# Optimization experiments

Hardware: AMD Instinct MI355X
Metric: run time of the kernel (lower is better)

Reference implementation:

```python
import jax, jax.numpy as jnp
import numpy as np
from jax import lax

B, T, C = 64, 1024, 256


def setup_inputs() -> dict:
    key = jax.random.key(0)
    k1, k2 = jax.random.split(key)
    sequences = jax.random.normal(k1, (B, T, C), dtype=jnp.float32)
    transitions = jax.random.normal(k2, (C, C), dtype=jnp.float32)
    return {"sequences": sequences, "transitions": transitions}


def _viterbi_decode(sequences, transitions):
    # sequences: [B, T, C] unary scores; transitions: [C_prev, C_cur]
    num_classes = sequences.shape[-1]
    emissions = jnp.swapaxes(sequences, 0, 1)  # [T, B, C]

    def fwd_step(alpha, emit):
        # alpha: [B, C_prev]; emit: [B, C_cur]
        m = alpha[:, :, None] + transitions[None, :, :]  # [B, C_prev, C_cur]
        bp = jnp.argmax(m, axis=1).astype(jnp.int32)     # [B, C_cur] backpointers
        new_alpha = jnp.max(m, axis=1) + emit            # [B, C_cur]
        return new_alpha, bp

    alpha, bps = lax.scan(fwd_step, emissions[0], emissions[1:])  # bps: [T-1, B, C]
    last_tag = jnp.argmax(alpha, axis=-1).astype(jnp.int32)       # [B]

    def back_step(tag, bp):
        # tag: [B] tag at t+1; bp: [B, C] backpointers computed at step t+1
        prev = jnp.take_along_axis(bp, tag[:, None], axis=1)[:, 0]
        return prev, prev

    _, tags = lax.scan(back_step, last_tag, bps, reverse=True)  # [T-1, B]
    full = jnp.concatenate([tags, last_tag[None, :]], axis=0)   # [T, B]
    return jnp.swapaxes(full, 0, 1)  # [B, T]


def reference(sequences, transitions):
    # Inference path of CRF.call: viterbi decode + one-hot over num_classes.
    tags = _viterbi_decode(sequences, transitions)
    return jax.nn.one_hot(tags, sequences.shape[-1], dtype=sequences.dtype)
```

## Files before the change

kernel.cpp:

```cpp
#include <hip/hip_runtime.h>

#define Bn 64
#define Tn 1024
#define Cn 256
#define TCROWS 127

typedef float nv4 __attribute__((ext_vector_type(4)));
__device__ __forceinline__ float4 nt_load4(const float* p) {
  nv4 r = __builtin_nontemporal_load((const nv4*)p);
  return make_float4(r.x, r.y, r.z, r.w);
}
__device__ __forceinline__ void nt_store4(float* p, float4 v) {
  nv4 r = {v.x, v.y, v.z, v.w};
  __builtin_nontemporal_store(r, (nv4*)p);
}

__device__ __forceinline__ float max3f(float a, float b, float c) {
  float d;
  asm("v_max3_f32 %0, %1, %2, %3" : "=v"(d) : "v"(a), "v"(b), "v"(c));
  return d;
}

template<int CTRL>
__device__ __forceinline__ float dpp_mov_f(float x) {
  return __int_as_float(__builtin_amdgcn_update_dpp(0, __float_as_int(x), CTRL, 0xF, 0xF, true));
}
template<int CTRL>
__device__ __forceinline__ void max_stage(float& v) {
  const float pv = __int_as_float(__builtin_amdgcn_update_dpp(
      (int)0xFF800000, __float_as_int(v), CTRL, 0xF, 0xF, false));
  v = fmaxf(v, pv);
}

__device__ __forceinline__ int argmax64_fast(float v, int i) {
  float mv = v;
  max_stage<0x111>(mv);
  max_stage<0x112>(mv);
  max_stage<0x114>(mv);
  max_stage<0x118>(mv);
  max_stage<0x142>(mv);
  max_stage<0x143>(mv);
  const float smax = __int_as_float(__builtin_amdgcn_readlane(__float_as_int(mv), 63));
  const unsigned long long m = __ballot(v == smax);
  const int ln = __ffsll((unsigned long long)m) - 1;
  return __builtin_amdgcn_readlane(i, ln);
}

__device__ __forceinline__ int apad(int m) { return (m >> 2) * 20 + (m & 3) * 4; }

#define REDUCE_CC(M, CMP)                                                     \
  {                                                                           \
    M = fmaxf(a0.x + tr4[0].CMP, a0.y + tr4[1].CMP);                          \
    M = max3f(M, a0.z + tr4[2].CMP, a0.w + tr4[3].CMP);                       \
    M = max3f(M, a1.x + tr4[4].CMP, a1.y + tr4[5].CMP);                       \
    M = max3f(M, a1.z + tr4[6].CMP, a1.w + tr4[7].CMP);                       \
    M = max3f(M, a2.x + tr4[8].CMP, a2.y + tr4[9].CMP);                       \
    M = max3f(M, a2.z + tr4[10].CMP, a2.w + tr4[11].CMP);                     \
    M = max3f(M, a3.x + tr4[12].CMP, a3.y + tr4[13].CMP);                     \
    M = max3f(M, a3.z + tr4[14].CMP, a3.w + tr4[15].CMP);                     \
  }

__global__ __launch_bounds__(1024, 4) void crf_fwd_kernel(
    float* __restrict__ seq, const float* __restrict__ trans,
    float* __restrict__ transT, int useT) {
  __shared__ float lds[64 * 65];
  const int bi = blockIdx.x;
  const int tid = threadIdx.x;

  if (bi < Bn) {
    float* sb = seq + (size_t)bi * (Tn * Cn);
    const int l = tid & 63;
    const int w = tid >> 6;
    const int c = l & 15;
    const int g = l >> 4;
    const int ccb = w * 16 + g * 4;
    const int cpb = c * 16;
    float4 tr4[16];
#pragma unroll
    for (int k = 0; k < 16; ++k)
      tr4[k] = *(const float4*)(trans + (size_t)(cpb + k) * Cn + ccb);

    float* ab0 = lds;
    float* ab1 = lds + 320;
    if (tid < 64) *(float4*)(ab0 + apad(tid)) = ((const float4*)sb)[tid];
    const bool leader = (c == 0);
    const int woff = apad(w * 4 + g);
    float4 e4, pna;
    if (leader) e4 = *(const float4*)(sb + Cn + ccb);
    __syncthreads();

    for (int t = 1; t < Tn; ++t) {
      const float* av = (t & 1) ? ab0 : ab1;
      float* aw = (t & 1) ? ab1 : ab0;
      const float* avc = av + c * 20;
      const float4 a0 = *(const float4*)(avc + 0);
      const float4 a1 = *(const float4*)(avc + 4);
      const float4 a2 = *(const float4*)(avc + 8);
      const float4 a3 = *(const float4*)(avc + 12);
      float4 pf;
      if (leader) {
        if (t > 1) *(float4*)(sb + (size_t)(t - 1) * Cn + ccb) = pna;
        const int tn = (t + 1 < Tn) ? (t + 1) : (Tn - 1);
        pf = *(const float4*)(sb + (size_t)tn * Cn + ccb);
      }
      float m0, m1, m2, m3;
      REDUCE_CC(m0, x)
      REDUCE_CC(m1, y)
      REDUCE_CC(m2, z)
      REDUCE_CC(m3, w)
      m0 = fmaxf(m0, dpp_mov_f<0x128>(m0)); m1 = fmaxf(m1, dpp_mov_f<0x128>(m1));
      m2 = fmaxf(m2, dpp_mov_f<0x128>(m2)); m3 = fmaxf(m3, dpp_mov_f<0x128>(m3));
      m0 = fmaxf(m0, dpp_mov_f<0x124>(m0)); m1 = fmaxf(m1, dpp_mov_f<0x124>(m1));
      m2 = fmaxf(m2, dpp_mov_f<0x124>(m2)); m3 = fmaxf(m3, dpp_mov_f<0x124>(m3));
      m0 = fmaxf(m0, dpp_mov_f<0x122>(m0)); m1 = fmaxf(m1, dpp_mov_f<0x122>(m1));
      m2 = fmaxf(m2, dpp_mov_f<0x122>(m2)); m3 = fmaxf(m3, dpp_mov_f<0x122>(m3));
      m0 = fmaxf(m0, dpp_mov_f<0x121>(m0)); m1 = fmaxf(m1, dpp_mov_f<0x121>(m1));
      m2 = fmaxf(m2, dpp_mov_f<0x121>(m2)); m3 = fmaxf(m3, dpp_mov_f<0x121>(m3));
      if (leader) {
        float4 na;
        na.x = m0 + e4.x; na.y = m1 + e4.y; na.z = m2 + e4.z; na.w = m3 + e4.w;
        *(float4*)(aw + woff) = na;
        pna = na;
        e4 = pf;
      }
      __syncthreads();
    }
    if (leader) *(float4*)(sb + (size_t)(Tn - 1) * Cn + ccb) = pna;
  } else if (useT) {
    const int idx = bi - Bn;
    const int ti = idx >> 2, tj = idx & 3;
    const int tx = tid & 63, ty = tid >> 6;
#pragma unroll
    for (int q = 0; q < 4; ++q) {
      const int row = q * 16 + ty;
      lds[tx * 65 + row] = trans[(size_t)(ti * 64 + row) * Cn + tj * 64 + tx];
    }
    __syncthreads();
#pragma unroll
    for (int q = 0; q < 4; ++q) {
      const int row = q * 16 + ty;
      transT[(size_t)(tj * 64 + row) * Cn + ti * 64 + tx] = lds[row * 65 + tx];
    }
  }
}

__device__ __forceinline__ float4 onehot4(int tg, int cp0) {
  float4 z;
  z.x = (tg == cp0 + 0) ? 1.0f : 0.0f; z.y = (tg == cp0 + 1) ? 1.0f : 0.0f;
  z.z = (tg == cp0 + 2) ? 1.0f : 0.0f; z.w = (tg == cp0 + 3) ? 1.0f : 0.0f;
  return z;
}

template<int K>
__device__ __forceinline__ int chain_chunk(
    const float* __restrict__ A, int* __restrict__ tags,
    const float* __restrict__ transT, const float* __restrict__ tc,
    int tag, int l) {
  const int cp0 = l * 4;
#pragma unroll
  for (int k = 0; k < K; ++k) {
    float4 tv;
    if (tag < TCROWS) {
      tv = *(const float4*)(tc + tag * Cn + cp0);
    } else {
      tv = *(const float4*)(transT + (size_t)tag * Cn + cp0);
    }
    const float4 ac = *(const float4*)(A + k * Cn + cp0);
    float v = ac.x + tv.x; int i = cp0;
    float vv; bool cnd;
    vv = ac.y + tv.y; cnd = vv > v; v = cnd ? vv : v; i = cnd ? cp0 + 1 : i;
    vv = ac.z + tv.z; cnd = vv > v; v = cnd ? vv : v; i = cnd ? cp0 + 2 : i;
    vv = ac.w + tv.w; cnd = vv > v; v = cnd ? vv : v; i = cnd ? cp0 + 3 : i;
    tag = argmax64_fast(v, i);
    if (l == 0) tags[k] = tag;
  }
  return tag;
}

__global__ __launch_bounds__(256) void crf_bwd_kernel(
    const float* __restrict__ seq, const float* __restrict__ trans,
    const float* __restrict__ transT, float* __restrict__ out, int useT) {
  __shared__ float aL[2][16][Cn];
  __shared__ float tc[TCROWS * Cn];
  __shared__ int tagL[2][16];
  const int b = blockIdx.x;
  const int tid = threadIdx.x;
  const int wv = tid >> 6;
  const int l = tid & 63;
  const int cp0 = l * 4;
  const float* sb = seq + (size_t)b * (Tn * Cn);
  float* ob = out + (size_t)b * (Tn * Cn);

  if (!useT) {
    if (wv == 0) {
      float4 a = *(const float4*)(sb + (size_t)(Tn - 1) * Cn + cp0);
      float v = a.x; int i = cp0; bool cnd;
      cnd = a.y > v; v = cnd ? a.y : v; i = cnd ? cp0 + 1 : i;
      cnd = a.z > v; v = cnd ? a.z : v; i = cnd ? cp0 + 2 : i;
      cnd = a.w > v; v = cnd ? a.w : v; i = cnd ? cp0 + 3 : i;
      int tag = argmax64_fast(v, i);
      *(float4*)(ob + (size_t)(Tn - 1) * Cn + cp0) = onehot4(tag, cp0);
      for (int t = Tn - 2; t >= 0; --t) {
        const float4 ac = *(const float4*)(sb + (size_t)t * Cn + cp0);
        float4 tv;
        tv.x = trans[(size_t)(cp0 + 0) * Cn + tag];
        tv.y = trans[(size_t)(cp0 + 1) * Cn + tag];
        tv.z = trans[(size_t)(cp0 + 2) * Cn + tag];
        tv.w = trans[(size_t)(cp0 + 3) * Cn + tag];
        float v2 = ac.x + tv.x; int i2 = cp0; float vv; bool c2;
        vv = ac.y + tv.y; c2 = vv > v2; v2 = c2 ? vv : v2; i2 = c2 ? cp0 + 1 : i2;
        vv = ac.z + tv.z; c2 = vv > v2; v2 = c2 ? vv : v2; i2 = c2 ? cp0 + 2 : i2;
        vv = ac.w + tv.w; c2 = vv > v2; v2 = c2 ? vv : v2; i2 = c2 ? cp0 + 3 : i2;
        tag = argmax64_fast(v2, i2);
        *(float4*)(ob + (size_t)t * Cn + cp0) = onehot4(tag, cp0);
      }
    }
    return;
  }

  {
    const int r0 = wv * 32;
    const int r1 = (r0 + 32 < TCROWS) ? (r0 + 32) : TCROWS;
    for (int r = r0; r < r1; ++r)
      *(float4*)(&tc[r * Cn + cp0]) = *(const float4*)(transT + (size_t)r * Cn + cp0);
  }

  int tag = 0;
  if (wv == 0) {
    float4 a = *(const float4*)(sb + (size_t)(Tn - 1) * Cn + cp0);
    float v = a.x; int i = cp0; bool cnd;
    cnd = a.y > v; v = cnd ? a.y : v; i = cnd ? cp0 + 1 : i;
    cnd = a.z > v; v = cnd ? a.z : v; i = cnd ? cp0 + 2 : i;
    cnd = a.w > v; v = cnd ? a.w : v; i = cnd ? cp0 + 3 : i;
    tag = argmax64_fast(v, i);
    *(float4*)(ob + (size_t)(Tn - 1) * Cn + cp0) = onehot4(tag, cp0);
  } else if (wv <= 2) {
    const int s0 = (wv == 1) ? 0 : 8, s1 = (wv == 1) ? 8 : 15;
    for (int s = s0; s < s1; ++s)
      *(float4*)(&aL[0][s][cp0]) = nt_load4(sb + (size_t)(1022 - s) * Cn + cp0);
  }
  __syncthreads();

  int p = 0, t0 = 1022, K = 15, pt0 = 0, pK = 0;
  for (int ch = 0; ch < 64; ++ch) {
    const int nt0 = t0 - K;
    if (wv == 0) {
      if (ch == 0) tag = chain_chunk<15>(&aL[p][0][0], tagL[p], transT, tc, tag, l);
      else        tag = chain_chunk<16>(&aL[p][0][0], tagL[p], transT, tc, tag, l);
    } else if (wv <= 2) {
      if (ch < 63) {
        const int s0 = (wv == 1) ? 0 : 8, s1 = (wv == 1) ? 8 : 16;
        for (int s = s0; s < s1; ++s)
          *(float4*)(&aL[1 - p][s][cp0]) = nt_load4(sb + (size_t)(nt0 - s) * Cn + cp0);
      }
    } else {
      if (ch > 0) {
        for (int k = 0; k < pK; ++k)
          nt_store4(ob + (size_t)(pt0 - k) * Cn + cp0, onehot4(tagL[1 - p][k], cp0));
      }
    }
    __syncthreads();
    pt0 = t0; pK = K; t0 = nt0; K = 16; p ^= 1;
  }
  if (wv == 3) {
    for (int k = 0; k < 16; ++k)
      nt_store4(ob + (size_t)(15 - k) * Cn + cp0, onehot4(tagL[1][k], cp0));
  }
}

extern "C" void kernel_launch(void* const* d_in, const int* in_sizes, int n_in,
                              void* d_out, int out_size, void* d_ws, size_t ws_size,
                              hipStream_t stream) {
  float* seq = (float*)d_in[0];
  const float* trans = (const float*)d_in[1];
  float* out = (float*)d_out;
  float* transT = (float*)d_ws;
  const int useT = (ws_size >= (size_t)Cn * Cn * sizeof(float)) ? 1 : 0;

  crf_fwd_kernel<<<dim3(Bn + 16), dim3(1024), 0, stream>>>(seq, trans, transT, useT);
  crf_bwd_kernel<<<dim3(Bn), dim3(256), 0, stream>>>(seq, trans, transT, out, useT);
}
```

Measured before the change: 1.255 ms.

## Replace per-step block barrier with LDS flag-based wave synchronization

The full-workgroup barrier at every time step of the forward recurrence is replaced by per-wave progress flags in LDS. Each wave publishes its step after its alpha write completes, and spins until all 16 producer waves have reached the previous step. This lets waves proceed without a global rendezvous, at the cost of spin-polling LDS and relying on the two-buffer ordering argument for correctness. The inline v_max3 asm is also replaced with plain fmaxf chains, leaving max fusion to the compiler.

```diff
diff --git a/kernel.cpp b/kernel.cpp
--- a/kernel.cpp
+++ b/kernel.cpp
@@ -13,12 +13,6 @@
 __device__ __forceinline__ void nt_store4(float* p, float4 v) {
   nv4 r = {v.x, v.y, v.z, v.w};
   __builtin_nontemporal_store(r, (nv4*)p);
-}
-
-__device__ __forceinline__ float max3f(float a, float b, float c) {
-  float d;
-  asm("v_max3_f32 %0, %1, %2, %3" : "=v"(d) : "v"(a), "v"(b), "v"(c));
-  return d;
 }
 
 template<int CTRL>
@@ -51,19 +45,20 @@
 #define REDUCE_CC(M, CMP)                                                     \
   {                                                                           \
     M = fmaxf(a0.x + tr4[0].CMP, a0.y + tr4[1].CMP);                          \
-    M = max3f(M, a0.z + tr4[2].CMP, a0.w + tr4[3].CMP);                       \
-    M = max3f(M, a1.x + tr4[4].CMP, a1.y + tr4[5].CMP);                       \
-    M = max3f(M, a1.z + tr4[6].CMP, a1.w + tr4[7].CMP);                       \
-    M = max3f(M, a2.x + tr4[8].CMP, a2.y + tr4[9].CMP);                       \
-    M = max3f(M, a2.z + tr4[10].CMP, a2.w + tr4[11].CMP);                     \
-    M = max3f(M, a3.x + tr4[12].CMP, a3.y + tr4[13].CMP);                     \
-    M = max3f(M, a3.z + tr4[14].CMP, a3.w + tr4[15].CMP);                     \
+    M = fmaxf(M, a0.z + tr4[2].CMP); M = fmaxf(M, a0.w + tr4[3].CMP);         \
+    M = fmaxf(M, a1.x + tr4[4].CMP); M = fmaxf(M, a1.y + tr4[5].CMP);         \
+    M = fmaxf(M, a1.z + tr4[6].CMP); M = fmaxf(M, a1.w + tr4[7].CMP);         \
+    M = fmaxf(M, a2.x + tr4[8].CMP); M = fmaxf(M, a2.y + tr4[9].CMP);         \
+    M = fmaxf(M, a2.z + tr4[10].CMP); M = fmaxf(M, a2.w + tr4[11].CMP);       \
+    M = fmaxf(M, a3.x + tr4[12].CMP); M = fmaxf(M, a3.y + tr4[13].CMP);       \
+    M = fmaxf(M, a3.z + tr4[14].CMP); M = fmaxf(M, a3.w + tr4[15].CMP);       \
   }
 
 __global__ __launch_bounds__(1024, 4) void crf_fwd_kernel(
     float* __restrict__ seq, const float* __restrict__ trans,
     float* __restrict__ transT, int useT) {
   __shared__ float lds[64 * 65];
+  __shared__ int flg[16];
   const int bi = blockIdx.x;
   const int tid = threadIdx.x;
 
@@ -83,6 +78,7 @@
     float* ab0 = lds;
     float* ab1 = lds + 320;
     if (tid < 64) *(float4*)(ab0 + apad(tid)) = ((const float4*)sb)[tid];
+    if (tid < 16) flg[tid] = 0;
     const bool leader = (c == 0);
     const int woff = apad(w * 4 + g);
     float4 e4, pna;
@@ -90,6 +86,12 @@
     __syncthreads();
 
     for (int t = 1; t < Tn; ++t) {
+      const int need = t - 1;
+      int fv;
+      do {
+        fv = __hip_atomic_load(&flg[c], __ATOMIC_ACQUIRE,
+                               __HIP_MEMORY_SCOPE_WORKGROUP);
+      } while (__any(fv < need));
       const float* av = (t & 1) ? ab0 : ab1;
       float* aw = (t & 1) ? ab1 : ab0;
       const float* avc = av + c * 20;
@@ -123,7 +125,10 @@
         pna = na;
         e4 = pf;
       }
-      __syncthreads();
+      asm volatile("s_waitcnt lgkmcnt(0)" ::: "memory");
+      if (leader)
+        __hip_atomic_store(&flg[w], t, __ATOMIC_RELAXED,
+                           __HIP_MEMORY_SCOPE_WORKGROUP);
     }
     if (leader) *(float4*)(sb + (size_t)(Tn - 1) * Cn + ccb) = pna;
   } else if (useT) {
```

Measured after the change: 1.598 ms. 27.3% more time.
